# Kernel tuning notes

Measured on AMD Instinct MI355X. Metric: run time of the kernel, lower is better.

The kernel has to match this reference:

```python
import jax, jax.numpy as jnp
import numpy as np

# Transformer_E (depth=1): Residual(PreNorm(MultiScaleRetention)) + Residual1(PreNorm1(FeedForward))
# MultiScaleRetention follows the standard RetNet parallel form, adapted to two inputs
# (Q from x, K/V from z) as implied by PreNorm passing both normed streams to fn.

B, S, DIM, HEADS, MLP = 16, 1024, 256, 4, 512
HEAD = DIM // HEADS  # per-head qkv size; v_dim = DIM
EPS = 1e-5           # torch LayerNorm/GroupNorm default eps


def _ln(x, w, b):
    mu = jnp.mean(x, -1, keepdims=True)
    var = jnp.mean((x - mu) ** 2, -1, keepdims=True)
    return (x - mu) * jax.lax.rsqrt(var + EPS) * w + b


def _decay_matrix():
    # RetNet gammas: 1 - exp(linspace(log(1/32), log(1/512), heads))
    gammas = 1.0 - jnp.exp(jnp.linspace(jnp.log(1.0 / 32.0), jnp.log(1.0 / 512.0), HEADS))
    n = jnp.arange(S)
    diff = (n[:, None] - n[None, :]).astype(jnp.float32)  # [S,S]
    causal = diff >= 0
    D = jnp.where(causal[None], gammas[:, None, None] ** diff[None], 0.0)  # [H,S,S]
    return D.astype(jnp.float32)


def setup_inputs() -> dict:
    key = jax.random.key(0)
    ks = jax.random.split(key, 9)
    s = 1.0 / DIM  # repo inits W as randn/hidden_size
    return {
        "x": jax.random.normal(ks[0], (B, S, DIM), jnp.float32),
        "y": jax.random.normal(ks[1], (B, S, DIM), jnp.float32),
        "ln1_w": jnp.ones((DIM,), jnp.float32),
        "ln1_b": jnp.zeros((DIM,), jnp.float32),
        "W_Q": jax.random.normal(ks[2], (HEADS, DIM, HEAD), jnp.float32) * s,
        "W_K": jax.random.normal(ks[3], (HEADS, DIM, HEAD), jnp.float32) * s,
        "W_V": jax.random.normal(ks[4], (HEADS, DIM, HEAD), jnp.float32) * s,
        "gn_w": jnp.ones((DIM,), jnp.float32),
        "gn_b": jnp.zeros((DIM,), jnp.float32),
        "W_G": jax.random.normal(ks[5], (DIM, DIM), jnp.float32) * s,
        "W_O": jax.random.normal(ks[6], (DIM, DIM), jnp.float32) * s,
        "ln2_w": jnp.ones((DIM,), jnp.float32),
        "ln2_b": jnp.zeros((DIM,), jnp.float32),
        "ff_w1": jax.random.normal(ks[7], (DIM, MLP), jnp.float32) * (DIM ** -0.5),
        "ff_b1": jnp.zeros((MLP,), jnp.float32),
        "ff_w2": jax.random.normal(ks[8], (MLP, DIM), jnp.float32) * (MLP ** -0.5),
        "ff_b2": jnp.zeros((DIM,), jnp.float32),
    }


def reference(x, y, ln1_w, ln1_b, W_Q, W_K, W_V, gn_w, gn_b, W_G, W_O,
              ln2_w, ln2_b, ff_w1, ff_b1, ff_w2, ff_b2):
    # PreNorm: x.real -> float (already real float32 here), shared LayerNorm on both streams
    xn = _ln(x, ln1_w, ln1_b)
    zn = _ln(y, ln1_w, ln1_b)

    # --- MultiScaleRetention (parallel form) ---
    Q = jnp.einsum('bsd,hde->bhse', xn, W_Q)
    K = jnp.einsum('bsd,hde->bhse', zn, W_K)
    V = jnp.einsum('bsd,hde->bhse', zn, W_V)
    D = _decay_matrix()                                       # [H,S,S] causal decay
    scores = jnp.einsum('bhne,bhme->bhnm', Q, K) * D[None]    # [B,H,S,S]
    Yh = jnp.einsum('bhnm,bhme->bhne', scores, V)             # [B,H,S,HEAD]

    # GroupNorm(heads, v_dim) applied token-wise: normalize each head slice
    mu = jnp.mean(Yh, -1, keepdims=True)
    var = jnp.mean((Yh - mu) ** 2, -1, keepdims=True)
    Yn = (Yh - mu) * jax.lax.rsqrt(var + EPS)
    Ycat = jnp.transpose(Yn, (0, 2, 1, 3)).reshape(x.shape[0], x.shape[1], DIM)
    Ycat = Ycat * gn_w + gn_b

    # swish gate + output projection
    g = xn @ W_G
    attn_out = ((g * jax.nn.sigmoid(g)) * Ycat) @ W_O

    x1 = attn_out + x                                         # Residual

    # --- FeedForward block (Residual1(PreNorm1(FFN))) ---
    x1n = _ln(x1, ln2_w, ln2_b)
    h = jax.nn.leaky_relu(x1n @ ff_w1 + ff_b1, negative_slope=0.01)
    ff = h @ ff_w2 + ff_b2
    return ff + x1
```

## Files before the change

kernel.cpp:

```cpp
#include <hip/hip_runtime.h>

typedef float f32x4 __attribute__((ext_vector_type(4)));
typedef short bf16x8 __attribute__((ext_vector_type(8)));

__device__ __forceinline__ unsigned short f2bf(float f) {
  unsigned int u = __builtin_bit_cast(unsigned int, f);
  u += 0x7fffu + ((u >> 16) & 1u);
  return (unsigned short)(u >> 16);
}
__device__ __forceinline__ float bf2f(unsigned short s) {
  unsigned int u = ((unsigned int)s) << 16;
  return __builtin_bit_cast(float, u);
}

__device__ __forceinline__ void gll16(const void* src, void* dst) {
  __builtin_amdgcn_global_load_lds((const __attribute__((address_space(1))) void*)src,
                                   (__attribute__((address_space(3))) void*)dst, 16, 0, 0);
}

__global__ __launch_bounds__(256) void pack_w(
    const float* __restrict__ WQ, const float* __restrict__ WK,
    const float* __restrict__ WV, const float* __restrict__ WG,
    const float* __restrict__ WO, const float* __restrict__ F1,
    const float* __restrict__ F2,
    unsigned short* __restrict__ qg, unsigned short* __restrict__ kv,
    unsigned short* __restrict__ wo, unsigned short* __restrict__ f1,
    unsigned short* __restrict__ f2)
{
  int i = blockIdx.x * 256 + threadIdx.x;
  if (i < 131072) {
    int n = i >> 8, d = i & 255;
    float v = (n < 256) ? WQ[((n >> 6) * 256 + d) * 64 + (n & 63)]
                        : WG[d * 256 + (n - 256)];
    qg[i] = f2bf(v);
  } else if (i < 262144) {
    int j = i - 131072; int n = j >> 8, d = j & 255;
    float v = (n < 256) ? WK[((n >> 6) * 256 + d) * 64 + (n & 63)]
                        : WV[(((n - 256) >> 6) * 256 + d) * 64 + ((n - 256) & 63)];
    kv[j] = f2bf(v);
  } else if (i < 327680) {
    int j = i - 262144; int n = j >> 8, d = j & 255;
    wo[j] = f2bf(WO[d * 256 + n]);
  } else if (i < 458752) {
    int j = i - 327680; int n = j >> 8, d = j & 255;
    f1[j] = f2bf(F1[d * 512 + n]);
  } else if (i < 589824) {
    int j = i - 458752; int n = j >> 9, k = j & 511;
    f2[j] = f2bf(F2[k * 256 + n]);
  }
}

__global__ __launch_bounds__(256) void ln_fwd(
    const float* __restrict__ X, const float* __restrict__ W,
    const float* __restrict__ Bv, unsigned short* __restrict__ Y)
{
  int lane = threadIdx.x & 63;
  size_t row = (size_t)blockIdx.x * 4 + (threadIdx.x >> 6);
  const float4 v = *reinterpret_cast<const float4*>(X + row * 256 + lane * 4);
  float s = v.x + v.y + v.z + v.w;
  #pragma unroll
  for (int off = 1; off < 64; off <<= 1) s += __shfl_xor(s, off);
  float mean = s * (1.0f / 256.0f);
  float dx = v.x - mean, dy = v.y - mean, dz = v.z - mean, dw = v.w - mean;
  float q = dx * dx + dy * dy + dz * dz + dw * dw;
  #pragma unroll
  for (int off = 1; off < 64; off <<= 1) q += __shfl_xor(q, off);
  float rstd = rsqrtf(q * (1.0f / 256.0f) + 1e-5f);
  float4 wv = *reinterpret_cast<const float4*>(W + lane * 4);
  float4 bv = *reinterpret_cast<const float4*>(Bv + lane * 4);
  ushort4 o;
  o.x = f2bf(dx * rstd * wv.x + bv.x);
  o.y = f2bf(dy * rstd * wv.y + bv.y);
  o.z = f2bf(dz * rstd * wv.z + bv.z);
  o.w = f2bf(dw * rstd * wv.w + bv.w);
  *reinterpret_cast<ushort4*>(Y + row * 256 + lane * 4) = o;
}

template<int EPI>
__global__ __launch_bounds__(256) void gemm_nt(
    const unsigned short* __restrict__ A, const unsigned short* __restrict__ Bw,
    int K, unsigned short* __restrict__ o0, unsigned short* __restrict__ o1,
    const float* __restrict__ bias, const float* __restrict__ resid,
    float* __restrict__ of)
{
  __shared__ __align__(16) char sA[128 * 128];
  __shared__ __align__(16) char sB[64 * 128];
  const int tid = threadIdx.x, lane = tid & 63, w = tid >> 6;
  const int flat = blockIdx.x + gridDim.x * blockIdx.y;
  const int c = flat & 7, jj = flat >> 3;
  const int m0 = (c * 16 + (jj & 15)) * 128;
  const int n0 = (jj >> 4) * 64;
  const int wr = (w >> 1) * 64, wc = (w & 1) * 32;
  const char* Ab = (const char*)A + (size_t)m0 * K * 2;
  const char* Bb = (const char*)Bw + (size_t)n0 * K * 2;
  const int srow = lane >> 3;
  const int soff = 16 * ((lane & 7) ^ srow);
  f32x4 acc[4][2] = {};

  for (int kt = 0; kt < K * 2; kt += 128) {
    #pragma unroll
    for (int p = 0; p < 4; ++p) {
      int row = p * 32 + w * 8 + srow;
      gll16(Ab + (size_t)row * (K * 2) + kt + soff, &sA[p * 4096 + w * 1024]);
    }
    #pragma unroll
    for (int p = 0; p < 2; ++p) {
      int row = p * 32 + w * 8 + srow;
      gll16(Bb + (size_t)row * (K * 2) + kt + soff, &sB[p * 4096 + w * 1024]);
    }
    asm volatile("s_waitcnt vmcnt(0)" ::: "memory");
    __syncthreads();
    #pragma unroll
    for (int kk = 0; kk < 2; ++kk) {
      const int ib = kk * 64 + ((lane >> 4) * 16);
      bf16x8 af[4], bfr[2];
      #pragma unroll
      for (int rf = 0; rf < 4; ++rf) {
        int row = wr + rf * 16 + (lane & 15);
        af[rf] = *reinterpret_cast<const bf16x8*>(sA + row * 128 + (ib ^ ((row & 7) << 4)));
      }
      #pragma unroll
      for (int cf = 0; cf < 2; ++cf) {
        int row = wc + cf * 16 + (lane & 15);
        bfr[cf] = *reinterpret_cast<const bf16x8*>(sB + row * 128 + (ib ^ ((row & 7) << 4)));
      }
      #pragma unroll
      for (int rf = 0; rf < 4; ++rf)
        #pragma unroll
        for (int cf = 0; cf < 2; ++cf)
          acc[rf][cf] = __builtin_amdgcn_mfma_f32_16x16x32_bf16(af[rf], bfr[cf], acc[rf][cf], 0, 0, 0);
    }
    __syncthreads();
  }

  #pragma unroll
  for (int rf = 0; rf < 4; ++rf) {
    #pragma unroll
    for (int cf = 0; cf < 2; ++cf) {
      const int r0 = m0 + wr + rf * 16 + ((lane >> 4) * 4);
      const int col = n0 + wc + cf * 16 + (lane & 15);
      f32x4 v = acc[rf][cf];
      if constexpr (EPI == 0) {
        unsigned short* dst = (n0 < 256) ? o0 : o1;
        int ccol = col & 255;
        #pragma unroll
        for (int j = 0; j < 4; ++j) dst[(size_t)(r0 + j) * 256 + ccol] = f2bf(v[j]);
      } else if constexpr (EPI == 1) {
        if (n0 < 256) {
          #pragma unroll
          for (int j = 0; j < 4; ++j) o0[(size_t)(r0 + j) * 256 + col] = f2bf(v[j]);
        } else {
          int vc = col - 256, hh = vc >> 6, e = vc & 63;
          int bh = (r0 >> 10) * 4 + hh, s0 = r0 & 1023;
          ushort4 pk;
          pk.x = f2bf(v[0]); pk.y = f2bf(v[1]); pk.z = f2bf(v[2]); pk.w = f2bf(v[3]);
          *reinterpret_cast<ushort4*>(o1 + (((size_t)bh * 64 + e) << 10) + s0) = pk;
        }
      } else if constexpr (EPI == 2) {
        #pragma unroll
        for (int j = 0; j < 4; ++j) {
          size_t idx = (size_t)(r0 + j) * 256 + col;
          of[idx] = v[j] + resid[idx];
        }
      } else if constexpr (EPI == 3) {
        float bc = bias[col];
        #pragma unroll
        for (int j = 0; j < 4; ++j) {
          float t = v[j] + bc;
          o0[(size_t)(r0 + j) * 512 + col] = f2bf(t >= 0.0f ? t : 0.01f * t);
        }
      } else {
        float bc = bias[col];
        #pragma unroll
        for (int j = 0; j < 4; ++j) {
          size_t idx = (size_t)(r0 + j) * 256 + col;
          of[idx] = v[j] + bc + resid[idx];
        }
      }
    }
  }
}

__global__ __launch_bounds__(256) void attn_ret(
    const unsigned short* __restrict__ Qb, const unsigned short* __restrict__ Kb,
    const unsigned short* __restrict__ Vt, const unsigned short* __restrict__ Gb,
    const float* __restrict__ gnw, const float* __restrict__ gnb,
    unsigned short* __restrict__ AY)
{
  __shared__ __align__(16) char sK[2][8192];
  __shared__ __align__(16) char sV[2][8192];
  __shared__ __align__(16) char sP[8192];
  const int tid = threadIdx.x, lane = tid & 63, w = tid >> 6;
  const int id = blockIdx.x;
  const int c = id & 7, jid = id >> 3;
  const int bh = c * 8 + (jid & 7);
  const int g = jid >> 3;
  const int qt = (g < 4) ? (15 - g) : (g < 8) ? (11 - g) : (g < 12) ? g : (g - 12);
  const int b = bh >> 2, h = bh & 3;

  const float la = logf(1.0f / 32.0f), lb = logf(1.0f / 512.0f);
  const float gamma = 1.0f - expf(la + (lb - la) * ((float)h * (1.0f / 3.0f)));
  const float lg = log2f(gamma);

  const char* Qg = (const char*)Qb
      + ((size_t)(b * 1024 + qt * 64 + w * 16 + (lane & 15))) * 512 + h * 128 + (lane >> 4) * 16;
  const bf16x8 aq0 = *reinterpret_cast<const bf16x8*>(Qg);
  const bf16x8 aq1 = *reinterpret_cast<const bf16x8*>(Qg + 64);

  const int nloc_b = w * 16 + ((lane >> 4) * 4);
  float Aj[4], Bcf[4];
  #pragma unroll
  for (int j = 0; j < 4; ++j) Aj[j] = exp2f((float)(qt * 64 + nloc_b + j) * lg);
  #pragma unroll
  for (int cf = 0; cf < 4; ++cf) Bcf[cf] = exp2f(-(float)(cf * 16 + (lane & 15)) * lg);
  const float g64 = exp2f(-64.0f * lg);

  const char* Kg = (const char*)Kb + ((size_t)(b * 1024)) * 512 + h * 128;
  const char* Vg = (const char*)Vt + ((size_t)bh * 64) * 2048;
  const int srow = lane >> 3;
  const int soff = 16 * ((lane & 7) ^ srow);

  auto stage = [&](int bufi, int t) {
    const char* kb = Kg + (size_t)(t * 64) * 512;
    const char* vb = Vg + (size_t)(t * 64) * 2;
    #pragma unroll
    for (int p = 0; p < 2; ++p) {
      int row = p * 32 + w * 8 + srow;
      gll16(kb + (size_t)row * 512 + soff, &sK[bufi][p * 4096 + w * 1024]);
      gll16(vb + (size_t)row * 2048 + soff, &sV[bufi][p * 4096 + w * 1024]);
    }
  };

  stage(0, 0);
  f32x4 o[4] = {};
  asm volatile("s_waitcnt vmcnt(0)" ::: "memory");
  __syncthreads();
  int buf = 0;

  for (int t = 0; t <= qt; ++t) {
    if (t < qt) stage(buf ^ 1, t + 1);

    f32x4 s4[4] = {};
    #pragma unroll
    for (int kk = 0; kk < 2; ++kk) {
      const int ib = kk * 64 + ((lane >> 4) * 16);
      const bf16x8 aq = kk ? aq1 : aq0;
      #pragma unroll
      for (int cf = 0; cf < 4; ++cf) {
        int kr = cf * 16 + (lane & 15);
        bf16x8 bk = *reinterpret_cast<const bf16x8*>(&sK[buf][kr * 128 + (ib ^ ((kr & 7) << 4))]);
        s4[cf] = __builtin_amdgcn_mfma_f32_16x16x32_bf16(aq, bk, s4[cf], 0, 0, 0);
      }
    }

    const bool diag = (t == qt);
    #pragma unroll
    for (int cf = 0; cf < 4; ++cf) {
      const int mloc = cf * 16 + (lane & 15);
      #pragma unroll
      for (int j = 0; j < 4; ++j) {
        float p = s4[cf][j] * (Aj[j] * Bcf[cf]);
        if (diag && (nloc_b + j - mloc) < 0) p = 0.0f;
        int pr = nloc_b + j;
        *reinterpret_cast<unsigned short*>(sP + pr * 128 + ((mloc * 2) ^ ((pr & 7) << 4))) = f2bf(p);
      }
    }

    #pragma unroll
    for (int kk = 0; kk < 2; ++kk) {
      const int ib = kk * 64 + ((lane >> 4) * 16);
      int pr = w * 16 + (lane & 15);
      bf16x8 ap = *reinterpret_cast<const bf16x8*>(sP + pr * 128 + (ib ^ ((pr & 7) << 4)));
      #pragma unroll
      for (int cf = 0; cf < 4; ++cf) {
        int vr = cf * 16 + (lane & 15);
        bf16x8 bv = *reinterpret_cast<const bf16x8*>(&sV[buf][vr * 128 + (ib ^ ((vr & 7) << 4))]);
        o[cf] = __builtin_amdgcn_mfma_f32_16x16x32_bf16(ap, bv, o[cf], 0, 0, 0);
      }
    }
    #pragma unroll
    for (int j = 0; j < 4; ++j) Aj[j] *= g64;

    asm volatile("s_waitcnt vmcnt(0)" ::: "memory");
    __syncthreads();
    buf ^= 1;
  }

  float gw[4], gb[4];
  #pragma unroll
  for (int cf = 0; cf < 4; ++cf) {
    int col = h * 64 + cf * 16 + (lane & 15);
    gw[cf] = gnw[col]; gb[cf] = gnb[col];
  }
  const int tokb = b * 1024 + qt * 64 + nloc_b;
  #pragma unroll
  for (int j = 0; j < 4; ++j) {
    float sm = 0.0f, sq = 0.0f;
    #pragma unroll
    for (int cf = 0; cf < 4; ++cf) { float xv = o[cf][j]; sm += xv; sq += xv * xv; }
    #pragma unroll
    for (int off = 1; off < 16; off <<= 1) { sm += __shfl_xor(sm, off); sq += __shfl_xor(sq, off); }
    float mean = sm * (1.0f / 64.0f);
    float var = sq * (1.0f / 64.0f) - mean * mean;
    float rstd = rsqrtf(var + 1e-5f);
    size_t tok = (size_t)(tokb + j);
    #pragma unroll
    for (int cf = 0; cf < 4; ++cf) {
      int col = h * 64 + cf * 16 + (lane & 15);
      float yn = (o[cf][j] - mean) * rstd * gw[cf] + gb[cf];
      float gv = bf2f(Gb[tok * 256 + col]);
      float sg = gv / (1.0f + expf(-gv));
      AY[tok * 256 + col] = f2bf(yn * sg);
    }
  }
}

extern "C" void kernel_launch(void* const* d_in, const int* in_sizes, int n_in,
                              void* d_out, int out_size, void* d_ws, size_t ws_size,
                              hipStream_t stream) {
  const float* x     = (const float*)d_in[0];
  const float* y     = (const float*)d_in[1];
  const float* ln1_w = (const float*)d_in[2];
  const float* ln1_b = (const float*)d_in[3];
  const float* W_Q   = (const float*)d_in[4];
  const float* W_K   = (const float*)d_in[5];
  const float* W_V   = (const float*)d_in[6];
  const float* gn_w  = (const float*)d_in[7];
  const float* gn_b  = (const float*)d_in[8];
  const float* W_G   = (const float*)d_in[9];
  const float* W_O   = (const float*)d_in[10];
  const float* ln2_w = (const float*)d_in[11];
  const float* ln2_b = (const float*)d_in[12];
  const float* ff_w1 = (const float*)d_in[13];
  const float* ff_b1 = (const float*)d_in[14];
  const float* ff_w2 = (const float*)d_in[15];
  const float* ff_b2 = (const float*)d_in[16];

  char* ws = (char*)d_ws;
  const size_t MB = 1048576;
  unsigned short* XN  = (unsigned short*)(ws + 0 * MB);
  unsigned short* ZN  = (unsigned short*)(ws + 8 * MB);
  unsigned short* QB  = (unsigned short*)(ws + 16 * MB);
  unsigned short* KB  = (unsigned short*)(ws + 24 * MB);
  unsigned short* VT  = (unsigned short*)(ws + 32 * MB);
  unsigned short* GB  = (unsigned short*)(ws + 40 * MB);
  unsigned short* WQG = (unsigned short*)(ws + 48 * MB);
  unsigned short* WKV = (unsigned short*)(ws + 48 * MB + 262144);
  unsigned short* WOp = (unsigned short*)(ws + 48 * MB + 524288);
  unsigned short* F1p = (unsigned short*)(ws + 48 * MB + 655360);
  unsigned short* F2p = (unsigned short*)(ws + 48 * MB + 917504);
  float*          X1  = (float*)(ws + 16 * MB);
  unsigned short* X1N = (unsigned short*)(ws + 32 * MB);
  unsigned short* H   = (unsigned short*)(ws + 0 * MB);
  unsigned short* AY  = ZN;
  float* out = (float*)d_out;

  pack_w<<<2304, 256, 0, stream>>>(W_Q, W_K, W_V, W_G, W_O, ff_w1, ff_w2,
                                   WQG, WKV, WOp, F1p, F2p);
  ln_fwd<<<4096, 256, 0, stream>>>(x, ln1_w, ln1_b, XN);
  ln_fwd<<<4096, 256, 0, stream>>>(y, ln1_w, ln1_b, ZN);
  gemm_nt<0><<<dim3(8, 128), 256, 0, stream>>>(XN, WQG, 256, QB, GB, nullptr, nullptr, nullptr);
  gemm_nt<1><<<dim3(8, 128), 256, 0, stream>>>(ZN, WKV, 256, KB, VT, nullptr, nullptr, nullptr);
  attn_ret<<<1024, 256, 0, stream>>>(QB, KB, VT, GB, gn_w, gn_b, AY);
  gemm_nt<2><<<dim3(4, 128), 256, 0, stream>>>(AY, WOp, 256, nullptr, nullptr, nullptr, x, X1);
  ln_fwd<<<4096, 256, 0, stream>>>(X1, ln2_w, ln2_b, X1N);
  gemm_nt<3><<<dim3(8, 128), 256, 0, stream>>>(X1N, F1p, 256, H, nullptr, ff_b1, nullptr, nullptr);
  gemm_nt<4><<<dim3(4, 128), 256, 0, stream>>>(H, F2p, 512, nullptr, nullptr, ff_b2, X1, out);
}
```

Baseline: 109.5 us.

## Fuse prep kernels, merge QKVG GEMMs, fuse Wo GEMM with LayerNorm, double-buffer

Folds both input LayerNorms into the weight-packing kernel and merges the Q/G and K/V projection GEMMs into one 3D-grid launch. The Wo projection now runs in a new kernel that covers the full 256-column rows, adds the residual and computes LayerNorm2 in its epilogue, which removes a separate LN pass and an fp32 round trip. All GEMMs gain double-buffered LDS staging so global loads overlap MFMA work. The cost is more LDS per block, which may lower occupancy, and LN2 now computes variance as E[x²]−mean², which is less numerically stable than the two-pass form.

```diff
diff --git a/kernel.cpp b/kernel.cpp
--- a/kernel.cpp
+++ b/kernel.cpp
@@ -18,16 +18,46 @@
                                    (__attribute__((address_space(3))) void*)dst, 16, 0, 0);
 }
 
-__global__ __launch_bounds__(256) void pack_w(
+__global__ __launch_bounds__(256) void prep(
+    const float* __restrict__ x, const float* __restrict__ y,
+    const float* __restrict__ ln1w, const float* __restrict__ ln1b,
     const float* __restrict__ WQ, const float* __restrict__ WK,
     const float* __restrict__ WV, const float* __restrict__ WG,
     const float* __restrict__ WO, const float* __restrict__ F1,
     const float* __restrict__ F2,
+    unsigned short* __restrict__ XN, unsigned short* __restrict__ ZN,
     unsigned short* __restrict__ qg, unsigned short* __restrict__ kv,
     unsigned short* __restrict__ wo, unsigned short* __restrict__ f1,
     unsigned short* __restrict__ f2)
 {
-  int i = blockIdx.x * 256 + threadIdx.x;
+  const int id = blockIdx.x;
+  if (id < 8192) {
+    const float* X = (id < 4096) ? x : y;
+    unsigned short* Y = (id < 4096) ? XN : ZN;
+    const int bid = id & 4095;
+    const int lane = threadIdx.x & 63;
+    const size_t row = (size_t)bid * 4 + (threadIdx.x >> 6);
+    const float4 v = *reinterpret_cast<const float4*>(X + row * 256 + lane * 4);
+    float s = v.x + v.y + v.z + v.w;
+    #pragma unroll
+    for (int off = 1; off < 64; off <<= 1) s += __shfl_xor(s, off);
+    float mean = s * (1.0f / 256.0f);
+    float dx = v.x - mean, dy = v.y - mean, dz = v.z - mean, dw = v.w - mean;
+    float q = dx * dx + dy * dy + dz * dz + dw * dw;
+    #pragma unroll
+    for (int off = 1; off < 64; off <<= 1) q += __shfl_xor(q, off);
+    float rstd = rsqrtf(q * (1.0f / 256.0f) + 1e-5f);
+    float4 wv = *reinterpret_cast<const float4*>(ln1w + lane * 4);
+    float4 bv = *reinterpret_cast<const float4*>(ln1b + lane * 4);
+    ushort4 o;
+    o.x = f2bf(dx * rstd * wv.x + bv.x);
+    o.y = f2bf(dy * rstd * wv.y + bv.y);
+    o.z = f2bf(dz * rstd * wv.z + bv.z);
+    o.w = f2bf(dw * rstd * wv.w + bv.w);
+    *reinterpret_cast<ushort4*>(Y + row * 256 + lane * 4) = o;
+    return;
+  }
+  int i = (id - 8192) * 256 + threadIdx.x;
   if (i < 131072) {
     int n = i >> 8, d = i & 255;
     float v = (n < 256) ? WQ[((n >> 6) * 256 + d) * 64 + (n & 63)]
@@ -50,66 +80,142 @@
   }
 }
 
-__global__ __launch_bounds__(256) void ln_fwd(
-    const float* __restrict__ X, const float* __restrict__ W,
-    const float* __restrict__ Bv, unsigned short* __restrict__ Y)
+__global__ __launch_bounds__(256) void gemm_qkvg(
+    const unsigned short* __restrict__ XN, const unsigned short* __restrict__ ZN,
+    const unsigned short* __restrict__ WQG, const unsigned short* __restrict__ WKV,
+    unsigned short* __restrict__ QB, unsigned short* __restrict__ GB,
+    unsigned short* __restrict__ KB, unsigned short* __restrict__ VT)
 {
-  int lane = threadIdx.x & 63;
-  size_t row = (size_t)blockIdx.x * 4 + (threadIdx.x >> 6);
-  const float4 v = *reinterpret_cast<const float4*>(X + row * 256 + lane * 4);
-  float s = v.x + v.y + v.z + v.w;
-  #pragma unroll
-  for (int off = 1; off < 64; off <<= 1) s += __shfl_xor(s, off);
-  float mean = s * (1.0f / 256.0f);
-  float dx = v.x - mean, dy = v.y - mean, dz = v.z - mean, dw = v.w - mean;
-  float q = dx * dx + dy * dy + dz * dz + dw * dw;
-  #pragma unroll
-  for (int off = 1; off < 64; off <<= 1) q += __shfl_xor(q, off);
-  float rstd = rsqrtf(q * (1.0f / 256.0f) + 1e-5f);
-  float4 wv = *reinterpret_cast<const float4*>(W + lane * 4);
-  float4 bv = *reinterpret_cast<const float4*>(Bv + lane * 4);
-  ushort4 o;
-  o.x = f2bf(dx * rstd * wv.x + bv.x);
-  o.y = f2bf(dy * rstd * wv.y + bv.y);
-  o.z = f2bf(dz * rstd * wv.z + bv.z);
-  o.w = f2bf(dw * rstd * wv.w + bv.w);
-  *reinterpret_cast<ushort4*>(Y + row * 256 + lane * 4) = o;
+  __shared__ __align__(16) char sA[2][16384];
+  __shared__ __align__(16) char sB[2][8192];
+  const int tid = threadIdx.x, lane = tid & 63, w = tid >> 6;
+  const int z = blockIdx.z;
+  const unsigned short* A = z ? ZN : XN;
+  const unsigned short* Bw = z ? WKV : WQG;
+  const int flat = blockIdx.x + 8 * blockIdx.y;
+  const int c = flat & 7, jj = flat >> 3;
+  const int m0 = (c * 16 + (jj & 15)) * 128;
+  const int n0 = (jj >> 4) * 64;
+  const int wr = (w >> 1) * 64, wc = (w & 1) * 32;
+  const char* Ab = (const char*)A + (size_t)m0 * 512;
+  const char* Bb = (const char*)Bw + (size_t)n0 * 512;
+  const int srow = lane >> 3;
+  const int soff = 16 * ((lane & 7) ^ srow);
+  f32x4 acc[4][2] = {};
+
+  auto stage = [&](int bufi, int kt) {
+    #pragma unroll
+    for (int p = 0; p < 4; ++p) {
+      int row = p * 32 + w * 8 + srow;
+      gll16(Ab + (size_t)row * 512 + kt + soff, &sA[bufi][p * 4096 + w * 1024]);
+    }
+    #pragma unroll
+    for (int p = 0; p < 2; ++p) {
+      int row = p * 32 + w * 8 + srow;
+      gll16(Bb + (size_t)row * 512 + kt + soff, &sB[bufi][p * 4096 + w * 1024]);
+    }
+  };
+
+  stage(0, 0);
+  asm volatile("s_waitcnt vmcnt(0)" ::: "memory");
+  __syncthreads();
+  int buf = 0;
+  for (int kt = 0; kt < 512; kt += 128) {
+    if (kt + 128 < 512) stage(buf ^ 1, kt + 128);
+    #pragma unroll
+    for (int kk = 0; kk < 2; ++kk) {
+      const int ib = kk * 64 + ((lane >> 4) * 16);
+      bf16x8 af[4], bfr[2];
+      #pragma unroll
+      for (int rf = 0; rf < 4; ++rf) {
+        int row = wr + rf * 16 + (lane & 15);
+        af[rf] = *reinterpret_cast<const bf16x8*>(&sA[buf][row * 128 + (ib ^ ((row & 7) << 4))]);
+      }
+      #pragma unroll
+      for (int cf = 0; cf < 2; ++cf) {
+        int row = wc + cf * 16 + (lane & 15);
+        bfr[cf] = *reinterpret_cast<const bf16x8*>(&sB[buf][row * 128 + (ib ^ ((row & 7) << 4))]);
+      }
+      #pragma unroll
+      for (int rf = 0; rf < 4; ++rf)
+        #pragma unroll
+        for (int cf = 0; cf < 2; ++cf)
+          acc[rf][cf] = __builtin_amdgcn_mfma_f32_16x16x32_bf16(af[rf], bfr[cf], acc[rf][cf], 0, 0, 0);
+    }
+    asm volatile("s_waitcnt vmcnt(0)" ::: "memory");
+    __syncthreads();
+    buf ^= 1;
+  }
+
+  #pragma unroll
+  for (int rf = 0; rf < 4; ++rf) {
+    #pragma unroll
+    for (int cf = 0; cf < 2; ++cf) {
+      const int r0 = m0 + wr + rf * 16 + ((lane >> 4) * 4);
+      const int col = n0 + wc + cf * 16 + (lane & 15);
+      f32x4 v = acc[rf][cf];
+      if (z == 0) {
+        unsigned short* dst = (n0 < 256) ? QB : GB;
+        int ccol = col & 255;
+        #pragma unroll
+        for (int j = 0; j < 4; ++j) dst[(size_t)(r0 + j) * 256 + ccol] = f2bf(v[j]);
+      } else {
+        if (n0 < 256) {
+          #pragma unroll
+          for (int j = 0; j < 4; ++j) KB[(size_t)(r0 + j) * 256 + col] = f2bf(v[j]);
+        } else {
+          int vc = col - 256, hh = vc >> 6, e = vc & 63;
+          int bh = (r0 >> 10) * 4 + hh, s0 = r0 & 1023;
+          ushort4 pk;
+          pk.x = f2bf(v[0]); pk.y = f2bf(v[1]); pk.z = f2bf(v[2]); pk.w = f2bf(v[3]);
+          *reinterpret_cast<ushort4*>(VT + (((size_t)bh * 64 + e) << 10) + s0) = pk;
+        }
+      }
+    }
+  }
 }
 
 template<int EPI>
 __global__ __launch_bounds__(256) void gemm_nt(
     const unsigned short* __restrict__ A, const unsigned short* __restrict__ Bw,
-    int K, unsigned short* __restrict__ o0, unsigned short* __restrict__ o1,
+    int K, unsigned short* __restrict__ o0,
     const float* __restrict__ bias, const float* __restrict__ resid,
     float* __restrict__ of)
 {
-  __shared__ __align__(16) char sA[128 * 128];
-  __shared__ __align__(16) char sB[64 * 128];
+  __shared__ __align__(16) char sA[2][16384];
+  __shared__ __align__(16) char sB[2][8192];
   const int tid = threadIdx.x, lane = tid & 63, w = tid >> 6;
   const int flat = blockIdx.x + gridDim.x * blockIdx.y;
   const int c = flat & 7, jj = flat >> 3;
   const int m0 = (c * 16 + (jj & 15)) * 128;
   const int n0 = (jj >> 4) * 64;
   const int wr = (w >> 1) * 64, wc = (w & 1) * 32;
-  const char* Ab = (const char*)A + (size_t)m0 * K * 2;
-  const char* Bb = (const char*)Bw + (size_t)n0 * K * 2;
+  const int K2 = K * 2;
+  const char* Ab = (const char*)A + (size_t)m0 * K2;
+  const char* Bb = (const char*)Bw + (size_t)n0 * K2;
   const int srow = lane >> 3;
   const int soff = 16 * ((lane & 7) ^ srow);
   f32x4 acc[4][2] = {};
 
-  for (int kt = 0; kt < K * 2; kt += 128) {
+  auto stage = [&](int bufi, int kt) {
     #pragma unroll
     for (int p = 0; p < 4; ++p) {
       int row = p * 32 + w * 8 + srow;
-      gll16(Ab + (size_t)row * (K * 2) + kt + soff, &sA[p * 4096 + w * 1024]);
+      gll16(Ab + (size_t)row * K2 + kt + soff, &sA[bufi][p * 4096 + w * 1024]);
     }
     #pragma unroll
     for (int p = 0; p < 2; ++p) {
       int row = p * 32 + w * 8 + srow;
-      gll16(Bb + (size_t)row * (K * 2) + kt + soff, &sB[p * 4096 + w * 1024]);
-    }
-    asm volatile("s_waitcnt vmcnt(0)" ::: "memory");
-    __syncthreads();
+      gll16(Bb + (size_t)row * K2 + kt + soff, &sB[bufi][p * 4096 + w * 1024]);
+    }
+  };
+
+  stage(0, 0);
+  asm volatile("s_waitcnt vmcnt(0)" ::: "memory");
+  __syncthreads();
+  int buf = 0;
+  for (int kt = 0; kt < K2; kt += 128) {
+    if (kt + 128 < K2) stage(buf ^ 1, kt + 128);
     #pragma unroll
     for (int kk = 0; kk < 2; ++kk) {
       const int ib = kk * 64 + ((lane >> 4) * 16);
@@ -117,12 +223,12 @@
       #pragma unroll
       for (int rf = 0; rf < 4; ++rf) {
         int row = wr + rf * 16 + (lane & 15);
-        af[rf] = *reinterpret_cast<const bf16x8*>(sA + row * 128 + (ib ^ ((row & 7) << 4)));
+        af[rf] = *reinterpret_cast<const bf16x8*>(&sA[buf][row * 128 + (ib ^ ((row & 7) << 4))]);
       }
       #pragma unroll
       for (int cf = 0; cf < 2; ++cf) {
         int row = wc + cf * 16 + (lane & 15);
-        bfr[cf] = *reinterpret_cast<const bf16x8*>(sB + row * 128 + (ib ^ ((row & 7) << 4)));
+        bfr[cf] = *reinterpret_cast<const bf16x8*>(&sB[buf][row * 128 + (ib ^ ((row & 7) << 4))]);
       }
       #pragma unroll
       for (int rf = 0; rf < 4; ++rf)
@@ -130,7 +236,9 @@
         for (int cf = 0; cf < 2; ++cf)
           acc[rf][cf] = __builtin_amdgcn_mfma_f32_16x16x32_bf16(af[rf], bfr[cf], acc[rf][cf], 0, 0, 0);
     }
+    asm volatile("s_waitcnt vmcnt(0)" ::: "memory");
     __syncthreads();
+    buf ^= 1;
   }
 
   #pragma unroll
@@ -140,29 +248,7 @@
       const int r0 = m0 + wr + rf * 16 + ((lane >> 4) * 4);
       const int col = n0 + wc + cf * 16 + (lane & 15);
       f32x4 v = acc[rf][cf];
-      if constexpr (EPI == 0) {
-        unsigned short* dst = (n0 < 256) ? o0 : o1;
-        int ccol = col & 255;
-        #pragma unroll
-        for (int j = 0; j < 4; ++j) dst[(size_t)(r0 + j) * 256 + ccol] = f2bf(v[j]);
-      } else if constexpr (EPI == 1) {
-        if (n0 < 256) {
-          #pragma unroll
-          for (int j = 0; j < 4; ++j) o0[(size_t)(r0 + j) * 256 + col] = f2bf(v[j]);
-        } else {
-          int vc = col - 256, hh = vc >> 6, e = vc & 63;
-          int bh = (r0 >> 10) * 4 + hh, s0 = r0 & 1023;
-          ushort4 pk;
-          pk.x = f2bf(v[0]); pk.y = f2bf(v[1]); pk.z = f2bf(v[2]); pk.w = f2bf(v[3]);
-          *reinterpret_cast<ushort4*>(o1 + (((size_t)bh * 64 + e) << 10) + s0) = pk;
-        }
-      } else if constexpr (EPI == 2) {
-        #pragma unroll
-        for (int j = 0; j < 4; ++j) {
-          size_t idx = (size_t)(r0 + j) * 256 + col;
-          of[idx] = v[j] + resid[idx];
-        }
-      } else if constexpr (EPI == 3) {
+      if constexpr (EPI == 3) {
         float bc = bias[col];
         #pragma unroll
         for (int j = 0; j < 4; ++j) {
@@ -176,6 +262,112 @@
           size_t idx = (size_t)(r0 + j) * 256 + col;
           of[idx] = v[j] + bc + resid[idx];
         }
+      }
+    }
+  }
+}
+
+__global__ __launch_bounds__(256) void gemm_wo_ln(
+    const unsigned short* __restrict__ AY, const unsigned short* __restrict__ WoT,
+    const float* __restrict__ x, const float* __restrict__ ln2w,
+    const float* __restrict__ ln2b,
+    float* __restrict__ X1, unsigned short* __restrict__ X1N)
+{
+  __shared__ __align__(16) char sA[2][4096];
+  __shared__ __align__(16) char sB[2][32768];
+  __shared__ float redS[32][4], redQ[32][4];
+  const int tid = threadIdx.x, lane = tid & 63, w = tid >> 6;
+  const int id = blockIdx.x;
+  const int c = id & 7, j5 = id >> 3;
+  const int m0 = (c * 64 + j5) * 32;
+  const char* Ab = (const char*)AY + (size_t)m0 * 512;
+  const char* Bb = (const char*)WoT;
+  const int srow = lane >> 3;
+  const int soff = 16 * ((lane & 7) ^ srow);
+  f32x4 acc[2][4] = {};
+
+  auto stage = [&](int bufi, int kt) {
+    {
+      int row = w * 8 + srow;
+      gll16(Ab + (size_t)row * 512 + kt + soff, &sA[bufi][w * 1024]);
+    }
+    #pragma unroll
+    for (int p = 0; p < 8; ++p) {
+      int row = w * 64 + p * 8 + srow;
+      gll16(Bb + (size_t)row * 512 + kt + soff, &sB[bufi][w * 8192 + p * 1024]);
+    }
+  };
+
+  stage(0, 0);
+  asm volatile("s_waitcnt vmcnt(0)" ::: "memory");
+  __syncthreads();
+  int buf = 0;
+  for (int kt = 0; kt < 512; kt += 128) {
+    if (kt + 128 < 512) stage(buf ^ 1, kt + 128);
+    #pragma unroll
+    for (int kk = 0; kk < 2; ++kk) {
+      const int ib = kk * 64 + ((lane >> 4) * 16);
+      bf16x8 af[2], bfr[4];
+      #pragma unroll
+      for (int mf = 0; mf < 2; ++mf) {
+        int row = mf * 16 + (lane & 15);
+        af[mf] = *reinterpret_cast<const bf16x8*>(&sA[buf][row * 128 + (ib ^ ((row & 7) << 4))]);
+      }
+      #pragma unroll
+      for (int nf = 0; nf < 4; ++nf) {
+        int row = w * 64 + nf * 16 + (lane & 15);
+        bfr[nf] = *reinterpret_cast<const bf16x8*>(&sB[buf][row * 128 + (ib ^ ((row & 7) << 4))]);
+      }
+      #pragma unroll
+      for (int mf = 0; mf < 2; ++mf)
+        #pragma unroll
+        for (int nf = 0; nf < 4; ++nf)
+          acc[mf][nf] = __builtin_amdgcn_mfma_f32_16x16x32_bf16(af[mf], bfr[nf], acc[mf][nf], 0, 0, 0);
+    }
+    asm volatile("s_waitcnt vmcnt(0)" ::: "memory");
+    __syncthreads();
+    buf ^= 1;
+  }
+
+  #pragma unroll
+  for (int mf = 0; mf < 2; ++mf) {
+    #pragma unroll
+    for (int j = 0; j < 4; ++j) {
+      const int rowg = m0 + mf * 16 + ((lane >> 4) * 4) + j;
+      float s = 0.0f, q = 0.0f;
+      #pragma unroll
+      for (int nf = 0; nf < 4; ++nf) {
+        const int col = w * 64 + nf * 16 + (lane & 15);
+        float v = acc[mf][nf][j] + x[(size_t)rowg * 256 + col];
+        acc[mf][nf][j] = v;
+        s += v; q += v * v;
+      }
+      #pragma unroll
+      for (int off = 1; off < 16; off <<= 1) { s += __shfl_xor(s, off); q += __shfl_xor(q, off); }
+      if ((lane & 15) == 0) {
+        int rl = mf * 16 + ((lane >> 4) * 4) + j;
+        redS[rl][w] = s; redQ[rl][w] = q;
+      }
+    }
+  }
+  __syncthreads();
+  #pragma unroll
+  for (int mf = 0; mf < 2; ++mf) {
+    #pragma unroll
+    for (int j = 0; j < 4; ++j) {
+      const int rl = mf * 16 + ((lane >> 4) * 4) + j;
+      const int rowg = m0 + rl;
+      float sm = redS[rl][0] + redS[rl][1] + redS[rl][2] + redS[rl][3];
+      float sq = redQ[rl][0] + redQ[rl][1] + redQ[rl][2] + redQ[rl][3];
+      float mean = sm * (1.0f / 256.0f);
+      float var = sq * (1.0f / 256.0f) - mean * mean;
+      float rstd = rsqrtf(var + 1e-5f);
+      #pragma unroll
+      for (int nf = 0; nf < 4; ++nf) {
+        const int col = w * 64 + nf * 16 + (lane & 15);
+        float v = acc[mf][nf][j];
+        X1[(size_t)rowg * 256 + col] = v;
+        X1N[(size_t)rowg * 256 + col] = f2bf((v - mean) * rstd * ln2w[col] + ln2b[col]);
       }
     }
   }
@@ -355,15 +547,11 @@
   unsigned short* AY  = ZN;
   float* out = (float*)d_out;
 
-  pack_w<<<2304, 256, 0, stream>>>(W_Q, W_K, W_V, W_G, W_O, ff_w1, ff_w2,
-                                   WQG, WKV, WOp, F1p, F2p);
-  ln_fwd<<<4096, 256, 0, stream>>>(x, ln1_w, ln1_b, XN);
-  ln_fwd<<<4096, 256, 0, stream>>>(y, ln1_w, ln1_b, ZN);
-  gemm_nt<0><<<dim3(8, 128), 256, 0, stream>>>(XN, WQG, 256, QB, GB, nullptr, nullptr, nullptr);
-  gemm_nt<1><<<dim3(8, 128), 256, 0, stream>>>(ZN, WKV, 256, KB, VT, nullptr, nullptr, nullptr);
+  prep<<<10496, 256, 0, stream>>>(x, y, ln1_w, ln1_b, W_Q, W_K, W_V, W_G, W_O,
+                                  ff_w1, ff_w2, XN, ZN, WQG, WKV, WOp, F1p, F2p);
+  gemm_qkvg<<<dim3(8, 128, 2), 256, 0, stream>>>(XN, ZN, WQG, WKV, QB, GB, KB, VT);
   attn_ret<<<1024, 256, 0, stream>>>(QB, KB, VT, GB, gn_w, gn_b, AY);
-  gemm_nt<2><<<dim3(4, 128), 256, 0, stream>>>(AY, WOp, 256, nullptr, nullptr, nullptr, x, X1);
-  ln_fwd<<<4096, 256, 0, stream>>>(X1, ln2_w, ln2_b, X1N);
-  gemm_nt<3><<<dim3(8, 128), 256, 0, stream>>>(X1N, F1p, 256, H, nullptr, ff_b1, nullptr, nullptr);
-  gemm_nt<4><<<dim3(4, 128), 256, 0, stream>>>(H, F2p, 512, nullptr, nullptr, ff_b2, X1, out);
-}
+  gemm_wo_ln<<<512, 256, 0, stream>>>(AY, WOp, x, ln2_w, ln2_b, X1, X1N);
+  gemm_nt<3><<<dim3(8, 128), 256, 0, stream>>>(X1N, F1p, 256, H, ff_b1, nullptr, nullptr);
+  gemm_nt<4><<<dim3(4, 128), 256, 0, stream>>>(H, F2p, 512, nullptr, ff_b2, X1, out);
+}
```

Result: faster. 100.5 us (-8.3%).
